# Performance work log

Measured on AMD Instinct MI355X. Metric: run time of the kernel, lower is better.

## Reference

```python
import jax, jax.numpy as jnp
import numpy as np

N_NODES = 50000
N_GRAPHS = 128
IN_DIM = 512
HID = 512
N_LAYERS = 3


def setup_inputs() -> dict:
    key = jax.random.key(0)
    ks = jax.random.split(key, 12)
    inp = {
        "x": jax.random.normal(ks[0], (N_NODES, IN_DIM), dtype=jnp.float32),
        "walk2": jax.random.randint(ks[1], (3, N_NODES), 0, N_NODES, dtype=jnp.int32),
        "walk3": jax.random.randint(ks[2], (4, N_NODES), 0, N_NODES, dtype=jnp.int32),
        "walk4": jax.random.randint(ks[3], (5, N_NODES), 0, N_NODES, dtype=jnp.int32),
        "batch": jnp.sort(jax.random.randint(ks[4], (N_NODES,), 0, N_GRAPHS, dtype=jnp.int32)),
    }
    dims = [IN_DIM, HID, HID]
    for i in range(N_LAYERS):
        scale = 1.0 / np.sqrt(dims[i])
        inp[f"W{i}"] = jax.random.normal(ks[5 + i], (dims[i], HID), dtype=jnp.float32) * scale
        inp[f"b{i}"] = jnp.zeros((HID,), dtype=jnp.float32)
    return inp


def _gather_sum(z, walk):
    # walk: [L, N] node indices -> sum of gathered embeddings, [N, H]
    L, N = walk.shape
    return jnp.take(z, walk.reshape(-1), axis=0).reshape(L, N, z.shape[1]).sum(0)


def reference(x, walk2, walk3, walk4, batch, W0, b0, W1, b1, W2, b2):
    layers = [(W0, b0), (W1, b1), (W2, b2)]
    path_batch = jnp.take(batch, walk2[0])  # [N]
    counts = jax.ops.segment_sum(jnp.ones((path_batch.shape[0],), jnp.float32),
                                 path_batch, num_segments=N_GRAPHS)
    denom = jnp.maximum(counts, 1.0)[:, None]  # avoid div-by-zero for empty graphs
    z = x
    g = []
    for W, b in layers:
        z = z @ W + b  # [N, H]
        path_emb = _gather_sum(z, walk2) + _gather_sum(z, walk3) + _gather_sum(z, walk4)
        pooled = jax.ops.segment_sum(path_emb, path_batch, num_segments=N_GRAPHS) / denom
        g.append(pooled)
    return jnp.concatenate(g, axis=1)  # [N_GRAPHS, 3*H]
```

## Files before the change

kernel.cpp:

```cpp
#include <hip/hip_runtime.h>

#define N_NODES 50000
#define N_GRAPHS 128
#define HID 512

#define KSPAN  416
#define KSPLIT 121
#define KPAD   (KSPAN * KSPLIT)
#define NPANEL (KPAD / 16)

#define C8_OFF     0
#define C8_BYTES   ((size_t)N_GRAPHS * KPAD)
#define PSUM_OFF   (C8_OFF + C8_BYTES)
#define PSUM_BYTES ((size_t)N_GRAPHS * HID * 4)
#define COUNTS_OFF (PSUM_OFF + PSUM_BYTES)
#define ZERO_BYTES (COUNTS_OFF + 512)
#define APACK_OFF  ZERO_BYTES
#define APACK_BYTES ((size_t)NPANEL * 4 * 64 * 16)
#define PART_OFF   (APACK_OFF + APACK_BYTES)
#define PART_BYTES ((size_t)KSPLIT * N_GRAPHS * HID * 4)

typedef __attribute__((ext_vector_type(8))) short bf16x8;
typedef __attribute__((ext_vector_type(16))) float f32x16;
typedef const __attribute__((address_space(1))) void* gas_t;
typedef __attribute__((address_space(3))) void* las_t;

__global__ __launch_bounds__(256)
void build_c_kernel(const int* __restrict__ w2, const int* __restrict__ w3,
                    const int* __restrict__ w4, const int* __restrict__ batch,
                    unsigned int* __restrict__ C32, int* __restrict__ counts) {
    __shared__ int hist[N_GRAPHS];
    const int t = threadIdx.x;
    if (t < N_GRAPHS) hist[t] = 0;
    __syncthreads();
    const int i = blockIdx.x * 256 + t;
    if (i < N_NODES) {
        const int a = w2[i];
        const int g = batch[a];
        atomicAdd(&hist[g], 1);
        unsigned int* row = C32 + (size_t)g * (KPAD / 4);
        int nn[12];
        nn[0]  = a;
        nn[1]  = w2[N_NODES + i];
        nn[2]  = w2[2 * N_NODES + i];
        nn[3]  = w3[i];
        nn[4]  = w3[N_NODES + i];
        nn[5]  = w3[2 * N_NODES + i];
        nn[6]  = w3[3 * N_NODES + i];
        nn[7]  = w4[i];
        nn[8]  = w4[N_NODES + i];
        nn[9]  = w4[2 * N_NODES + i];
        nn[10] = w4[3 * N_NODES + i];
        nn[11] = w4[4 * N_NODES + i];
#pragma unroll
        for (int j = 0; j < 12; ++j) {
            const int nd = nn[j];
            atomicAdd(&row[nd >> 2], 1u << ((nd & 3) * 8));
        }
    }
    __syncthreads();
    if (t < N_GRAPHS) { const int hv = hist[t]; if (hv) atomicAdd(&counts[t], hv); }
}

__device__ inline unsigned pack_bf16(unsigned a, unsigned b) {
    return (__builtin_bit_cast(unsigned, (float)a) >> 16) |
           (__builtin_bit_cast(unsigned, (float)b) & 0xFFFF0000u);
}

__global__ __launch_bounds__(256)
void c8_to_apack_kernel(const unsigned char* __restrict__ C8,
                        uint4* __restrict__ Apack) {
    const int kp = blockIdx.x;
    const int t = threadIdx.x;
    const int mt = t >> 6;
    const int l = t & 63;
    const int row = mt * 32 + (l & 31);
    const int k0 = kp * 16 + 8 * (l >> 5);
    const uint2 b = *(const uint2*)(C8 + (size_t)row * KPAD + k0);
    uint4 o;
    o.x = pack_bf16(b.x & 0xFFu, (b.x >> 8) & 0xFFu);
    o.y = pack_bf16((b.x >> 16) & 0xFFu, b.x >> 24);
    o.z = pack_bf16(b.y & 0xFFu, (b.y >> 8) & 0xFFu);
    o.w = pack_bf16((b.y >> 16) & 0xFFu, b.y >> 24);
    Apack[(size_t)(kp * 4 + mt) * 64 + l] = o;
}

template <int ATOMIC>
__global__ __launch_bounds__(256, 4)
void pool_gemm3_kernel(const float* __restrict__ x,
                       const uint4* __restrict__ Apack,
                       float* __restrict__ dst) {
    __shared__ float lbuf[32 * 64];
    const int t = threadIdx.x;
    const int lane = t & 63;
    const int w = t >> 6;
    const int n = lane & 31;
    const int h = lane >> 5;
    const int nt = w & 1;
    const int p = w >> 1;
    const int colbase = blockIdx.x * 64;
    const int ks = blockIdx.y;
    const int kbase = ks * KSPAN;

    f32x16 acc0, acc1;
#pragma unroll
    for (int r = 0; r < 16; ++r) { acc0[r] = 0.f; acc1[r] = 0.f; }

    for (int ch = 0; ch < KSPAN / 32; ++ch) {
        const int k0 = kbase + ch * 32;
        if (k0 >= N_NODES) break;
        if (k0 + 32 <= N_NODES) {
#pragma unroll
            for (int i = 0; i < 2; ++i) {
                const int r = w * 8 + i * 4 + (lane >> 4);
                const float* gp = x + (size_t)(k0 + r) * HID + colbase + (lane & 15) * 4;
                las_t lp = (las_t)&lbuf[(w * 8 + i * 4) * 64];
                __builtin_amdgcn_global_load_lds((gas_t)gp, lp, 16, 0, 0);
            }
        } else {
#pragma unroll
            for (int j = 0; j < 8; ++j) {
                const int idx = t + j * 256;
                const int r = idx >> 6, c = idx & 63;
                const int kg = k0 + r;
                lbuf[idx] = (kg < N_NODES) ? x[(size_t)kg * HID + colbase + c] : 0.f;
            }
        }
        __syncthreads();

        const int kp0 = k0 >> 4;
#pragma unroll
        for (int kk = 0; kk < 2; ++kk) {
            unsigned bw[4];
#pragma unroll
            for (int j2 = 0; j2 < 4; ++j2) {
                const int kl = kk * 16 + 8 * h + 2 * j2;
                const unsigned u0 = __builtin_bit_cast(unsigned, lbuf[kl * 64 + nt * 32 + n]);
                const unsigned u1 = __builtin_bit_cast(unsigned, lbuf[(kl + 1) * 64 + nt * 32 + n]);
                bw[j2] = (u0 >> 16) | (u1 & 0xFFFF0000u);
            }
            const uint4 bu = make_uint4(bw[0], bw[1], bw[2], bw[3]);
            const bf16x8 bf = __builtin_bit_cast(bf16x8, bu);
            const bf16x8 a0 = __builtin_bit_cast(bf16x8,
                Apack[(size_t)((kp0 + kk) * 4 + 2 * p) * 64 + lane]);
            const bf16x8 a1 = __builtin_bit_cast(bf16x8,
                Apack[(size_t)((kp0 + kk) * 4 + 2 * p + 1) * 64 + lane]);
            acc0 = __builtin_amdgcn_mfma_f32_32x32x16_bf16(a0, bf, acc0, 0, 0, 0);
            acc1 = __builtin_amdgcn_mfma_f32_32x32x16_bf16(a1, bf, acc1, 0, 0, 0);
        }
        __syncthreads();
    }

    float* outp = ATOMIC ? dst : dst + (size_t)ks * (N_GRAPHS * HID);
    const int col = colbase + nt * 32 + n;
#pragma unroll
    for (int r = 0; r < 16; ++r) {
        const int row0 = 2 * p * 32 + (r & 3) + 8 * (r >> 2) + 4 * h;
        if (ATOMIC) {
            atomicAdd(&outp[(size_t)row0 * HID + col], acc0[r]);
            atomicAdd(&outp[(size_t)(row0 + 32) * HID + col], acc1[r]);
        } else {
            outp[(size_t)row0 * HID + col] = acc0[r];
            outp[(size_t)(row0 + 32) * HID + col] = acc1[r];
        }
    }
}

__global__ __launch_bounds__(256)
void reduce_part_kernel(const float* __restrict__ part, float* __restrict__ Psum) {
    const int id = blockIdx.x * 256 + threadIdx.x;
    float s0 = 0.f, s1 = 0.f, s2 = 0.f, s3 = 0.f;
    int k = 0;
    for (; k + 4 <= KSPLIT; k += 4) {
        s0 += part[(size_t)k * (N_GRAPHS * HID) + id];
        s1 += part[(size_t)(k + 1) * (N_GRAPHS * HID) + id];
        s2 += part[(size_t)(k + 2) * (N_GRAPHS * HID) + id];
        s3 += part[(size_t)(k + 3) * (N_GRAPHS * HID) + id];
    }
    for (; k < KSPLIT; ++k) s0 += part[(size_t)k * (N_GRAPHS * HID) + id];
    Psum[id] = (s0 + s1) + (s2 + s3);
}

__global__ __launch_bounds__(256)
void layer_gemm_kernel(const float* __restrict__ A, int lda, int scaleA,
                       const float* __restrict__ W,
                       const float* __restrict__ bias,
                       const int* __restrict__ counts,
                       float* __restrict__ out) {
    __shared__ float Alds[16][128];
    const int ct = blockIdx.x, rt = blockIdx.y, ksb = blockIdx.z;
    const int t = threadIdx.x;
    const int cc = ct * 64 + (t & 63);
    const int wv = t >> 6;
    const int k0 = ksb * 128;

    for (int idx = t; idx < 16 * 32; idx += 256) {
        const int rr = idx >> 5;
        const int kk = (idx & 31) * 4;
        const int row = rt * 16 + rr;
        float4 v = *(const float4*)&A[(size_t)row * lda + k0 + kk];
        if (scaleA) {
            const float inv = 1.f / (float)max(counts[row], 1);
            v.x *= inv; v.y *= inv; v.z *= inv; v.w *= inv;
        }
        *(float4*)&Alds[rr][kk] = v;
    }
    __syncthreads();

    const int r0 = rt * 16 + wv * 4;
    float a0 = 0.f, a1 = 0.f, a2 = 0.f, a3 = 0.f;
#pragma unroll 8
    for (int k = 0; k < 128; ++k) {
        const float wval = W[(size_t)(k0 + k) * HID + cc];
        a0 += Alds[wv * 4 + 0][k] * wval;
        a1 += Alds[wv * 4 + 1][k] * wval;
        a2 += Alds[wv * 4 + 2][k] * wval;
        a3 += Alds[wv * 4 + 3][k] * wval;
    }
    if (ksb == 0) {
        const float bc = bias[cc];
        a0 += (counts[r0 + 0] > 0 ? 12.f : 0.f) * bc;
        a1 += (counts[r0 + 1] > 0 ? 12.f : 0.f) * bc;
        a2 += (counts[r0 + 2] > 0 ? 12.f : 0.f) * bc;
        a3 += (counts[r0 + 3] > 0 ? 12.f : 0.f) * bc;
    }
    atomicAdd(&out[(size_t)(r0 + 0) * 1536 + cc], a0);
    atomicAdd(&out[(size_t)(r0 + 1) * 1536 + cc], a1);
    atomicAdd(&out[(size_t)(r0 + 2) * 1536 + cc], a2);
    atomicAdd(&out[(size_t)(r0 + 3) * 1536 + cc], a3);
}

extern "C" void kernel_launch(void* const* d_in, const int* in_sizes, int n_in,
                              void* d_out, int out_size, void* d_ws, size_t ws_size,
                              hipStream_t stream) {
    const float* x     = (const float*)d_in[0];
    const int*   w2    = (const int*)d_in[1];
    const int*   w3    = (const int*)d_in[2];
    const int*   w4    = (const int*)d_in[3];
    const int*   batch = (const int*)d_in[4];
    const float* W0    = (const float*)d_in[5];
    const float* b0    = (const float*)d_in[6];
    const float* W1    = (const float*)d_in[7];
    const float* b1    = (const float*)d_in[8];
    const float* W2    = (const float*)d_in[9];
    const float* b2    = (const float*)d_in[10];
    float* out = (float*)d_out;

    unsigned char* ws  = (unsigned char*)d_ws;
    unsigned int* C32  = (unsigned int*)(ws + C8_OFF);
    float* Psum        = (float*)(ws + PSUM_OFF);
    int* counts        = (int*)(ws + COUNTS_OFF);
    uint4* Apack       = (uint4*)(ws + APACK_OFF);
    float* part        = (float*)(ws + PART_OFF);
    const bool use_part = ws_size >= PART_OFF + PART_BYTES;

    hipMemsetAsync(d_ws, 0, ZERO_BYTES, stream);
    hipMemsetAsync(d_out, 0, (size_t)out_size * 4, stream);

    build_c_kernel<<<(N_NODES + 255) / 256, 256, 0, stream>>>(w2, w3, w4, batch, C32, counts);
    c8_to_apack_kernel<<<NPANEL, 256, 0, stream>>>((const unsigned char*)C32, Apack);

    if (use_part) {
        pool_gemm3_kernel<0><<<dim3(8, KSPLIT), 256, 0, stream>>>(x, Apack, part);
        reduce_part_kernel<<<256, 256, 0, stream>>>(part, Psum);
    } else {
        pool_gemm3_kernel<1><<<dim3(8, KSPLIT), 256, 0, stream>>>(x, Apack, Psum);
    }

    layer_gemm_kernel<<<dim3(8, 8, 4), 256, 0, stream>>>(Psum, HID, 1, W0, b0, counts, out);
    layer_gemm_kernel<<<dim3(8, 8, 4), 256, 0, stream>>>(out, 1536, 0, W1, b1, counts, out + 512);
    layer_gemm_kernel<<<dim3(8, 8, 4), 256, 0, stream>>>(out + 512, 1536, 0, W2, b2, counts, out + 1024);
}
```

Baseline: 279.6 us.

## Enlarge pooling GEMM tile to 128 columns and 128-row K chunks with 512 threads

The pooling GEMM block now covers 128 output columns with 8 waves instead of 64 columns with 4 waves. It stages 128-row K chunks (64 KB LDS) per barrier rather than 32 rows, and each block spans 512 K rows, cutting KSPLIT from 121 to 98. This halves how often each Apack panel is re-read across column blocks, reduces barrier count per MFMA, and shrinks the partial buffer the reduction must sum. In exchange the block needs 64 KB of LDS, which lowers occupancy, and the grid drops to 392 blocks, which may underfill the GPU.

New measurement: 276.4 us. No clear change (-1.2%).

```diff
diff --git a/kernel.cpp b/kernel.cpp
--- a/kernel.cpp
+++ b/kernel.cpp
@@ -4,8 +4,8 @@
 #define N_GRAPHS 128
 #define HID 512
 
-#define KSPAN  416
-#define KSPLIT 121
+#define KSPAN  512
+#define KSPLIT 98
 #define KPAD   (KSPAN * KSPLIT)
 #define NPANEL (KPAD / 16)
 
@@ -86,19 +86,19 @@
 }
 
 template <int ATOMIC>
-__global__ __launch_bounds__(256, 4)
-void pool_gemm3_kernel(const float* __restrict__ x,
+__global__ __launch_bounds__(512, 4)
+void pool_gemm4_kernel(const float* __restrict__ x,
                        const uint4* __restrict__ Apack,
                        float* __restrict__ dst) {
-    __shared__ float lbuf[32 * 64];
+    __shared__ float lbuf[128 * 128];
     const int t = threadIdx.x;
     const int lane = t & 63;
     const int w = t >> 6;
     const int n = lane & 31;
     const int h = lane >> 5;
-    const int nt = w & 1;
-    const int p = w >> 1;
-    const int colbase = blockIdx.x * 64;
+    const int nt = w & 3;
+    const int mh = w >> 2;
+    const int colbase = blockIdx.x * 128;
     const int ks = blockIdx.y;
     const int kbase = ks * KSPAN;
 
@@ -106,22 +106,23 @@
 #pragma unroll
     for (int r = 0; r < 16; ++r) { acc0[r] = 0.f; acc1[r] = 0.f; }
 
-    for (int ch = 0; ch < KSPAN / 32; ++ch) {
-        const int k0 = kbase + ch * 32;
+    for (int ch = 0; ch < 4; ++ch) {
+        const int k0 = kbase + ch * 128;
         if (k0 >= N_NODES) break;
-        if (k0 + 32 <= N_NODES) {
-#pragma unroll
-            for (int i = 0; i < 2; ++i) {
-                const int r = w * 8 + i * 4 + (lane >> 4);
-                const float* gp = x + (size_t)(k0 + r) * HID + colbase + (lane & 15) * 4;
-                las_t lp = (las_t)&lbuf[(w * 8 + i * 4) * 64];
+        if (k0 + 128 <= N_NODES) {
+#pragma unroll
+            for (int i = 0; i < 8; ++i) {
+                const int rbase = w * 16 + 2 * i;
+                const float* gp = x + (size_t)(k0 + rbase + (lane >> 5)) * HID
+                                    + colbase + (lane & 31) * 4;
+                las_t lp = (las_t)&lbuf[rbase * 128];
                 __builtin_amdgcn_global_load_lds((gas_t)gp, lp, 16, 0, 0);
             }
         } else {
 #pragma unroll
-            for (int j = 0; j < 8; ++j) {
-                const int idx = t + j * 256;
-                const int r = idx >> 6, c = idx & 63;
+            for (int j = 0; j < 32; ++j) {
+                const int idx = t + j * 512;
+                const int r = idx >> 7, c = idx & 127;
                 const int kg = k0 + r;
                 lbuf[idx] = (kg < N_NODES) ? x[(size_t)kg * HID + colbase + c] : 0.f;
             }
@@ -130,21 +131,21 @@
 
         const int kp0 = k0 >> 4;
 #pragma unroll
-        for (int kk = 0; kk < 2; ++kk) {
+        for (int s = 0; s < 8; ++s) {
             unsigned bw[4];
 #pragma unroll
             for (int j2 = 0; j2 < 4; ++j2) {
-                const int kl = kk * 16 + 8 * h + 2 * j2;
-                const unsigned u0 = __builtin_bit_cast(unsigned, lbuf[kl * 64 + nt * 32 + n]);
-                const unsigned u1 = __builtin_bit_cast(unsigned, lbuf[(kl + 1) * 64 + nt * 32 + n]);
+                const int kl = s * 16 + 8 * h + 2 * j2;
+                const unsigned u0 = __builtin_bit_cast(unsigned, lbuf[kl * 128 + nt * 32 + n]);
+                const unsigned u1 = __builtin_bit_cast(unsigned, lbuf[(kl + 1) * 128 + nt * 32 + n]);
                 bw[j2] = (u0 >> 16) | (u1 & 0xFFFF0000u);
             }
             const uint4 bu = make_uint4(bw[0], bw[1], bw[2], bw[3]);
             const bf16x8 bf = __builtin_bit_cast(bf16x8, bu);
             const bf16x8 a0 = __builtin_bit_cast(bf16x8,
-                Apack[(size_t)((kp0 + kk) * 4 + 2 * p) * 64 + lane]);
+                Apack[(size_t)((kp0 + s) * 4 + 2 * mh) * 64 + lane]);
             const bf16x8 a1 = __builtin_bit_cast(bf16x8,
-                Apack[(size_t)((kp0 + kk) * 4 + 2 * p + 1) * 64 + lane]);
+                Apack[(size_t)((kp0 + s) * 4 + 2 * mh + 1) * 64 + lane]);
             acc0 = __builtin_amdgcn_mfma_f32_32x32x16_bf16(a0, bf, acc0, 0, 0, 0);
             acc1 = __builtin_amdgcn_mfma_f32_32x32x16_bf16(a1, bf, acc1, 0, 0, 0);
         }
@@ -155,7 +156,7 @@
     const int col = colbase + nt * 32 + n;
 #pragma unroll
     for (int r = 0; r < 16; ++r) {
-        const int row0 = 2 * p * 32 + (r & 3) + 8 * (r >> 2) + 4 * h;
+        const int row0 = mh * 64 + (r & 3) + 8 * (r >> 2) + 4 * h;
         if (ATOMIC) {
             atomicAdd(&outp[(size_t)row0 * HID + col], acc0[r]);
             atomicAdd(&outp[(size_t)(row0 + 32) * HID + col], acc1[r]);
@@ -169,16 +170,12 @@
 __global__ __launch_bounds__(256)
 void reduce_part_kernel(const float* __restrict__ part, float* __restrict__ Psum) {
     const int id = blockIdx.x * 256 + threadIdx.x;
-    float s0 = 0.f, s1 = 0.f, s2 = 0.f, s3 = 0.f;
-    int k = 0;
-    for (; k + 4 <= KSPLIT; k += 4) {
+    float s0 = 0.f, s1 = 0.f;
+    for (int k = 0; k + 2 <= KSPLIT; k += 2) {
         s0 += part[(size_t)k * (N_GRAPHS * HID) + id];
         s1 += part[(size_t)(k + 1) * (N_GRAPHS * HID) + id];
-        s2 += part[(size_t)(k + 2) * (N_GRAPHS * HID) + id];
-        s3 += part[(size_t)(k + 3) * (N_GRAPHS * HID) + id];
-    }
-    for (; k < KSPLIT; ++k) s0 += part[(size_t)k * (N_GRAPHS * HID) + id];
-    Psum[id] = (s0 + s1) + (s2 + s3);
+    }
+    Psum[id] = s0 + s1;
 }
 
 __global__ __launch_bounds__(256)
@@ -261,10 +258,10 @@
     c8_to_apack_kernel<<<NPANEL, 256, 0, stream>>>((const unsigned char*)C32, Apack);
 
     if (use_part) {
-        pool_gemm3_kernel<0><<<dim3(8, KSPLIT), 256, 0, stream>>>(x, Apack, part);
+        pool_gemm4_kernel<0><<<dim3(4, KSPLIT), 512, 0, stream>>>(x, Apack, part);
         reduce_part_kernel<<<256, 256, 0, stream>>>(part, Psum);
     } else {
-        pool_gemm3_kernel<1><<<dim3(8, KSPLIT), 256, 0, stream>>>(x, Apack, Psum);
+        pool_gemm4_kernel<1><<<dim3(4, KSPLIT), 512, 0, stream>>>(x, Apack, Psum);
     }
 
     layer_gemm_kernel<<<dim3(8, 8, 4), 256, 0, stream>>>(Psum, HID, 1, W0, b0, counts, out);
```
